# Kernel tuning notes

Measured on AMD Instinct MI355X. Metric: run time of the kernel, lower is better.

The kernel has to match this reference:

```python
import jax, jax.numpy as jnp
import numpy as np

B, N = 16, 63
Np1 = N + 1
M = Np1 * Np1
NB_LABELS = 8
NB_EDGE_LABELS = 4


def _sinkhorn(S, n_iter):
    # LSAPE eps-assignment: alternately normalize rows/cols, leaving the
    # epsilon (last) row/col unnormalized since it may absorb many nodes.
    inner = jnp.arange(Np1) < N
    def step(S, _):
        S = jnp.where(inner[None, :, None], S / S.sum(2, keepdims=True), S)
        S = jnp.where(inner[None, None, :], S / S.sum(1, keepdims=True), S)
        return S, None
    S, _ = jax.lax.scan(step, S, None, length=n_iter)
    return S


def _forward(node_weighs, edge_weighs, A1, A2, l1, l2):
    cn = jax.nn.relu(node_weighs)
    ce = jax.nn.relu(edge_weighs)
    node_ins_del, edge_ins_del = cn[-1], ce[-1]
    iu = jnp.triu_indices(NB_LABELS, k=1)
    node_costs = jnp.zeros((NB_LABELS, NB_LABELS), cn.dtype).at[iu].set(cn[:-1])
    node_costs = node_costs + node_costs.T
    ie = jnp.triu_indices(NB_EDGE_LABELS, k=1)
    edge_costs = jnp.zeros((NB_EDGE_LABELS, NB_EDGE_LABELS), ce.dtype).at[ie].set(ce[:-1])
    edge_costs = edge_costs + edge_costs.T
    E1 = NB_EDGE_LABELS + 1
    # pairwise edge-cost lookup table T[a,b], a,b in {0..E}, 0 = no edge.
    # substitution added twice, matching add_ followed by C = C + ... in source.
    T = jnp.zeros((E1, E1), ce.dtype)
    T = T.at[1:, 1:].set(2.0 * edge_costs)
    T = T.at[0, 1:].set(edge_ins_del)
    T = T.at[1:, 0].set(edge_ins_del)
    # pad adjacency with the epsilon row/col of zeros
    A1p = jnp.pad(A1, ((0, 0), (0, 1), (0, 1)))
    A2p = jnp.pad(A2, ((0, 0), (0, 1), (0, 1)))
    # Dmat[b, u*Np1+v, i*Np1+l] = T[A1p[b,u,i], A2p[b,v,l]]  (quadratic edge term)
    idx = A1p[:, :, None, :, None] * E1 + A2p[:, None, :, None, :]
    Dmat = T.reshape(-1)[idx.reshape(B, M, M)]
    dia = jnp.arange(M)
    Dmat = Dmat.at[:, dia, dia].set(0.0)  # C - eye*diag(C)
    # linear node-cost vector c (diagonal of C): substitution on the N x N
    # block, nodeInsDel on epsilon row/col, 0 at (eps,eps).
    nc = node_costs[l1[:, :, None], l2[:, None, :]]
    cmat = jnp.full((B, Np1, Np1), node_ins_del, node_weighs.dtype)
    cmat = cmat.at[:, :N, :N].set(nc)
    cmat = cmat.at[:, N, N].set(0.0)
    c = cmat.reshape(B, M)
    # eps-assignment init (10 Sinkhorn iters), then Frank-Wolfe (15 iters,
    # 5 Sinkhorn iters per LAP solve), matching franck_wolfe(x0, D, c, 5, 15, n, m).
    x0 = _sinkhorn(jnp.exp(-cmat), 10).reshape(B, M)
    def fw_step(x, _):
        g = c + jnp.einsum('bpq,bq->bp', Dmat, x)
        b = _sinkhorn(jnp.exp(-g.reshape(B, Np1, Np1)), 5).reshape(B, M)
        d = b - x
        den = jnp.einsum('bp,bpq,bq->b', d, Dmat, d)
        num = jnp.einsum('bp,bp->b', d, g)
        t = jnp.where(den > 0.0,
                      jnp.clip(-num / jnp.where(den > 0.0, den, 1.0), 0.0, 1.0),
                      (num < 0.0).astype(x.dtype))
        return x + t[:, None] * d, None
    x, _ = jax.lax.scan(fw_step, x0, None, length=15)
    ged = 0.5 * jnp.einsum('bp,bpq,bq->b', x, Dmat, x) + jnp.einsum('bp,bp->b', c, x)
    return (ged - ged.min()) / (ged.max() - ged.min())


def _sym_adj(key):
    lab = jax.random.randint(key, (B, N, N), 0, NB_EDGE_LABELS + 1)
    keep = jax.random.uniform(jax.random.fold_in(key, 1), (B, N, N)) < 0.15
    A = jnp.triu(lab * keep, 1)
    return (A + jnp.transpose(A, (0, 2, 1))).astype(jnp.int32)


def setup_inputs() -> dict:
    key = jax.random.key(0)
    k = jax.random.split(key, 6)
    n_pairs = NB_LABELS * (NB_LABELS - 1) // 2
    e_pairs = NB_EDGE_LABELS * (NB_EDGE_LABELS - 1) // 2
    base = 1.0 / (n_pairs + e_pairs + 2)
    return {
        'node_weighs': base + 0.001 * jax.random.uniform(k[0], (n_pairs + 1,), jnp.float32),
        'edge_weighs': base + 0.001 * jax.random.uniform(k[1], (e_pairs + 1,), jnp.float32),
        'A1': _sym_adj(k[2]),
        'A2': _sym_adj(k[3]),
        'l1': jax.random.randint(k[4], (B, N), 0, NB_LABELS).astype(jnp.int32),
        'l2': jax.random.randint(k[5], (B, N), 0, NB_LABELS).astype(jnp.int32),
    }


def reference(node_weighs, edge_weighs, A1, A2, l1, l2):
    return _forward(node_weighs, edge_weighs, A1, A2, l1, l2)
```

## Files before the change

### kernel.cpp

```cpp
#include <hip/hip_runtime.h>
#include <math.h>

#define NBATCH 16
#define NN 63

typedef __attribute__((ext_vector_type(8))) short short8;
typedef __attribute__((ext_vector_type(4))) float f32x4;

__device__ __forceinline__ unsigned short f2bf(float f) {
    unsigned int u = __float_as_uint(f);
    u += 0x7fffu + ((u >> 16) & 1u);
    return (unsigned short)(u >> 16);
}

template <int CTRL>
__device__ __forceinline__ float dpp_add(float s) {
    int si = __builtin_bit_cast(int, s);
    int t  = __builtin_amdgcn_update_dpp(si, si, CTRL, 0xF, 0xF, true);
    return s + __builtin_bit_cast(float, t);
}
__device__ __forceinline__ float red8_dpp(float s) {
    s = dpp_add<0xB1>(s);
    s = dpp_add<0x4E>(s);
    s = dpp_add<0x141>(s);
    return s;
}

__global__ __launch_bounds__(512) void ged_kernel(
    const float* __restrict__ node_w, const float* __restrict__ edge_w,
    const int* __restrict__ A1g, const int* __restrict__ A2g,
    const int* __restrict__ l1g, const int* __restrict__ l2g,
    float* __restrict__ ged_out)
{
    const int b    = blockIdx.x;
    const int tid  = threadIdx.x;
    const int lane = tid & 63;
    const int w    = tid >> 6;
    const int lr   = lane & 15;
    const int lg   = lane >> 4;

    __shared__ __align__(16) float XK[64*65];
    __shared__ __align__(16) unsigned short Xb[4096];
    __shared__ __align__(16) unsigned short Rb[4][4096];
    __shared__ __align__(16) unsigned short Wb[4][4096];
    __shared__ __align__(16) unsigned short I1b[4][4096];
    __shared__ __align__(16) float rX[64];
    __shared__ __align__(16) float us[64];
    __shared__ __align__(16) float vs[64];
    __shared__ __align__(16) float red[16];
    __shared__ float ncost[64];
    __shared__ unsigned short Qbf[20];
    __shared__ float cns[29], ces[7];
    __shared__ float deg2f[64];
    __shared__ int l1s[64], l2s[64];

    if (tid < 29) cns[tid] = fmaxf(node_w[tid], 0.f);
    else if (tid >= 32 && tid < 39) ces[tid-32] = fmaxf(edge_w[tid-32], 0.f);
    if (tid >= 64 && tid < 128) l1s[tid-64] = (tid-64 < NN) ? l1g[b*NN + tid-64] : 0;
    else if (tid >= 128 && tid < 192) l2s[tid-128] = (tid-128 < NN) ? l2g[b*NN + tid-128] : 0;
    __syncthreads();
    if (tid < 64) {
        int r0 = tid >> 3, c1 = tid & 7;
        float vv = 0.f;
        if (r0 != c1) {
            int lo = min(r0, c1), hi = max(r0, c1);
            vv = cns[lo*7 - (lo*(lo-1))/2 + (hi-lo-1)];
        }
        ncost[tid] = vv;
    } else if (tid < 80) {
        int a = (tid-64) >> 2, b2 = tid & 3;
        float ec = 0.f;
        if (a != b2) {
            int lo = min(a, b2), hi = max(a, b2);
            ec = ces[lo*3 - (lo*(lo-1))/2 + (hi-lo-1)];
        }
        Qbf[a*5 + b2 + 1] = f2bf(2.f*ec - 2.f*ces[6]);
    } else if (tid < 84) {
        Qbf[(tid-80)*5] = 0;
    }
    __syncthreads();
    #pragma unroll
    for (int r = 0; r < 8; ++r) {
        int row = w + (r << 3);
        int v2 = 0, v1 = 0;
        if (row < NN && lane < NN) {
            v2 = A2g[((size_t)b*NN + row)*NN + lane];
            v1 = A1g[((size_t)b*NN + row)*NN + lane];
        }
        int T = row >> 4, lrr = row & 15;
        int kc = lane >> 5, lgg = (lane >> 3) & 3, e = lane & 7;
        int ci = ((((T<<1)+kc)*4 + lgg)*16 + lrr)*8 + e;
        Wb[0][ci] = Qbf[ 0 + v2];
        Wb[1][ci] = Qbf[ 5 + v2];
        Wb[2][ci] = Qbf[10 + v2];
        Wb[3][ci] = Qbf[15 + v2];
        unsigned long long mv = __ballot(v2 != 0);
        if (lane == 0) deg2f[row] = (float)__popcll(mv);
        I1b[0][ci] = (v1 == 1) ? 0x3F80 : 0;
        I1b[1][ci] = (v1 == 2) ? 0x3F80 : 0;
        I1b[2][ci] = (v1 == 3) ? 0x3F80 : 0;
        I1b[3][ci] = (v1 == 4) ? 0x3F80 : 0;
    }
    __syncthreads();

    const float eid = ces[6];
    const float nid = cns[28];

    int i0s[2], jcs[2], rts[2], cts[2];
    float ed2s[2];
    #pragma unroll
    for (int s = 0; s < 2; ++s) {
        int t = w + (s << 3);
        rts[s] = t >> 2; cts[s] = t & 3;
        i0s[s] = rts[s]*16 + lg*4;
        jcs[s] = cts[s]*16 + lr;
        ed2s[s] = eid * deg2f[jcs[s]];
    }

    float c_reg[2][4];
    #pragma unroll
    for (int s = 0; s < 2; ++s)
        #pragma unroll
        for (int r = 0; r < 4; ++r) {
            int i = i0s[s] + r, j = jcs[s];
            c_reg[s][r] = (i < NN && j < NN) ? ncost[(l1s[i] << 3) + l2s[j]]
                          : ((i == NN && j == NN) ? 0.f : nid);
        }

    const int q8  = tid & 7;
    const int rr8 = tid >> 3;
    const int c8  = q8 << 3;
    float Krow[8], Kcol[8];

    auto expK = [&](float (*gv)[4]) {
        #pragma unroll
        for (int s = 0; s < 2; ++s)
            #pragma unroll
            for (int r = 0; r < 4; ++r)
                XK[(i0s[s] + r)*65 + jcs[s]] = __expf(-gv[s][r]);
        __syncthreads();
    };

    auto sink8 = [&](int iters) {
        #pragma unroll
        for (int u = 0; u < 8; ++u) {
            Krow[u] = XK[rr8*65 + c8 + u];
            Kcol[u] = XK[(c8+u)*65 + rr8];
        }
        float s0 = ((Krow[0]+Krow[1])+(Krow[2]+Krow[3]))+((Krow[4]+Krow[5])+(Krow[6]+Krow[7]));
        s0 = red8_dpp(s0);
        if (q8 == 0) us[rr8] = (rr8 < NN) ? __builtin_amdgcn_rcpf(s0) : 1.f;
        __syncthreads();
        for (int it = 0; it < iters; ++it) {
            {
                float4 ua = *(const float4*)&us[c8], ub = *(const float4*)&us[c8+4];
                float t = ((Kcol[0]*ua.x + Kcol[1]*ua.y) + (Kcol[2]*ua.z + Kcol[3]*ua.w))
                        + ((Kcol[4]*ub.x + Kcol[5]*ub.y) + (Kcol[6]*ub.z + Kcol[7]*ub.w));
                t = red8_dpp(t);
                if (q8 == 0) vs[rr8] = (rr8 < NN) ? __builtin_amdgcn_rcpf(t) : 1.f;
            }
            __syncthreads();
            if (it + 1 < iters) {
                float4 va = *(const float4*)&vs[c8], vb = *(const float4*)&vs[c8+4];
                float t = ((Krow[0]*va.x + Krow[1]*va.y) + (Krow[2]*va.z + Krow[3]*va.w))
                        + ((Krow[4]*vb.x + Krow[5]*vb.y) + (Krow[6]*vb.z + Krow[7]*vb.w));
                t = red8_dpp(t);
                if (q8 == 0) us[rr8] = (rr8 < NN) ? __builtin_amdgcn_rcpf(t) : 1.f;
                __syncthreads();
            }
        }
    };

    auto fin8 = [&]() {
        float4 va = *(const float4*)&vs[c8], vb = *(const float4*)&vs[c8+4];
        float uR = us[rr8];
        float p[8];
        p[0]=Krow[0]*va.x; p[1]=Krow[1]*va.y; p[2]=Krow[2]*va.z; p[3]=Krow[3]*va.w;
        p[4]=Krow[4]*vb.x; p[5]=Krow[5]*vb.y; p[6]=Krow[6]*vb.z; p[7]=Krow[7]*vb.w;
        float sr = red8_dpp(((p[0]+p[1])+(p[2]+p[3])) + ((p[4]+p[5])+(p[6]+p[7])));
        short8 xs;
        #pragma unroll
        for (int u = 0; u < 8; ++u) {
            float xv = uR * p[u];
            XK[rr8*65 + c8 + u] = xv;
            xs[u] = (short)f2bf(xv);
        }
        int ci = (((((rr8>>4)<<1) + (q8>>2))*4 + (q8&3))*16 + (rr8&15)) << 3;
        *(short8*)&Xb[ci] = xs;
        if (q8 == 0) rX[rr8] = uR * sr;
        __syncthreads();
    };

    auto M1R = [&]() {
        #pragma unroll
        for (int s = 0; s < 2; ++s) {
            const int rt = rts[s], ct = cts[s];
            f32x4 P0 = {0.f,0.f,0.f,0.f}, P1 = P0, P2 = P0, P3 = P0;
            #pragma unroll
            for (int kc = 0; kc < 2; ++kc) {
                const int ai = ((((rt<<1)+kc)*4 + lg)*16 + lr) << 3;
                const int bi = ((((ct<<1)+kc)*4 + lg)*16 + lr) << 3;
                short8 af = *(const short8*)&Xb[ai];
                P0 = __builtin_amdgcn_mfma_f32_16x16x32_bf16(af, *(const short8*)&Wb[0][bi], P0, 0,0,0);
                P1 = __builtin_amdgcn_mfma_f32_16x16x32_bf16(af, *(const short8*)&Wb[1][bi], P1, 0,0,0);
                P2 = __builtin_amdgcn_mfma_f32_16x16x32_bf16(af, *(const short8*)&Wb[2][bi], P2, 0,0,0);
                P3 = __builtin_amdgcn_mfma_f32_16x16x32_bf16(af, *(const short8*)&Wb[3][bi], P3, 0,0,0);
            }
            float4 rx4 = *(const float4*)&rX[i0s[s]];
            P0[0] += eid*rx4.x; P0[1] += eid*rx4.y; P0[2] += eid*rx4.z; P0[3] += eid*rx4.w;
            P1[0] += eid*rx4.x; P1[1] += eid*rx4.y; P1[2] += eid*rx4.z; P1[3] += eid*rx4.w;
            P2[0] += eid*rx4.x; P2[1] += eid*rx4.y; P2[2] += eid*rx4.z; P2[3] += eid*rx4.w;
            P3[0] += eid*rx4.x; P3[1] += eid*rx4.y; P3[2] += eid*rx4.z; P3[3] += eid*rx4.w;
            const int cw = (((ct<<1) + (rt>>1))*4 + ((rt&1)*2 + (lg>>1)))*16 + lr;
            const int si = (cw << 3) + ((lg & 1) << 2);
            {
                unsigned long long v =  (unsigned long long)(f2bf(P0[0]) | ((unsigned)f2bf(P0[1])<<16))
                                     | ((unsigned long long)(f2bf(P0[2]) | ((unsigned)f2bf(P0[3])<<16)) << 32);
                *(unsigned long long*)&Rb[0][si] = v;
            }
            {
                unsigned long long v =  (unsigned long long)(f2bf(P1[0]) | ((unsigned)f2bf(P1[1])<<16))
                                     | ((unsigned long long)(f2bf(P1[2]) | ((unsigned)f2bf(P1[3])<<16)) << 32);
                *(unsigned long long*)&Rb[1][si] = v;
            }
            {
                unsigned long long v =  (unsigned long long)(f2bf(P2[0]) | ((unsigned)f2bf(P2[1])<<16))
                                     | ((unsigned long long)(f2bf(P2[2]) | ((unsigned)f2bf(P2[3])<<16)) << 32);
                *(unsigned long long*)&Rb[2][si] = v;
            }
            {
                unsigned long long v =  (unsigned long long)(f2bf(P3[0]) | ((unsigned)f2bf(P3[1])<<16))
                                     | ((unsigned long long)(f2bf(P3[2]) | ((unsigned)f2bf(P3[3])<<16)) << 32);
                *(unsigned long long*)&Rb[3][si] = v;
            }
        }
        __syncthreads();
    };

    auto M2 = [&](float (*out)[4]) {
        #pragma unroll
        for (int s = 0; s < 2; ++s) {
            const int rt = rts[s], ct = cts[s];
            f32x4 acc = {0.f,0.f,0.f,0.f};
            #pragma unroll
            for (int kc = 0; kc < 2; ++kc) {
                const int ai = ((((rt<<1)+kc)*4 + lg)*16 + lr) << 3;
                const int bi = ((((ct<<1)+kc)*4 + lg)*16 + lr) << 3;
                #pragma unroll
                for (int a = 0; a < 4; ++a) {
                    short8 af = *(const short8*)&I1b[a][ai];
                    short8 bf = *(const short8*)&Rb[a][bi];
                    acc = __builtin_amdgcn_mfma_f32_16x16x32_bf16(af, bf, acc, 0,0,0);
                }
            }
            #pragma unroll
            for (int r = 0; r < 4; ++r) out[s][r] = acc[r] + ed2s[s];
        }
    };

    expK(c_reg);
    sink8(10);
    fin8();
    M1R();
    float x[2][4], dx[2][4], bb[2][4], gvv[2][4];
    M2(dx);
    #pragma unroll
    for (int s = 0; s < 2; ++s)
        #pragma unroll
        for (int r = 0; r < 4; ++r)
            x[s][r] = XK[(i0s[s] + r)*65 + jcs[s]];

    for (int it = 0; it < 15; ++it) {
        #pragma unroll
        for (int s = 0; s < 2; ++s)
            #pragma unroll
            for (int r = 0; r < 4; ++r)
                gvv[s][r] = c_reg[s][r] + dx[s][r];
        expK(gvv);
        sink8(5);
        fin8();
        M1R();
        float db[2][4];
        M2(db);
        #pragma unroll
        for (int s = 0; s < 2; ++s)
            #pragma unroll
            for (int r = 0; r < 4; ++r)
                bb[s][r] = XK[(i0s[s] + r)*65 + jcs[s]];
        float dn = 0.f, nm = 0.f;
        #pragma unroll
        for (int s = 0; s < 2; ++s)
            #pragma unroll
            for (int r = 0; r < 4; ++r) {
                float d = bb[s][r] - x[s][r];
                dn += d * (db[s][r] - dx[s][r]);
                nm += d * gvv[s][r];
            }
        dn = red8_dpp(dn);  nm = red8_dpp(nm);
        dn += __shfl_xor(dn, 8, 64);  nm += __shfl_xor(nm, 8, 64);
        dn += __shfl_xor(dn, 16, 64); nm += __shfl_xor(nm, 16, 64);
        dn += __shfl_xor(dn, 32, 64); nm += __shfl_xor(nm, 32, 64);
        if (lane == 0) { red[w] = dn; red[8 + w] = nm; }
        __syncthreads();
        float4 pa = *(const float4*)&red[0], pb = *(const float4*)&red[4];
        float4 pc = *(const float4*)&red[8], pd = *(const float4*)&red[12];
        float den = (pa.x+pa.y+pa.z+pa.w) + (pb.x+pb.y+pb.z+pb.w);
        float num = (pc.x+pc.y+pc.z+pc.w) + (pd.x+pd.y+pd.z+pd.w);
        float t;
        if (den > 0.f) t = fminf(fmaxf(-num / den, 0.f), 1.f);
        else           t = (num < 0.f) ? 1.f : 0.f;
        #pragma unroll
        for (int s = 0; s < 2; ++s)
            #pragma unroll
            for (int r = 0; r < 4; ++r) {
                float d = bb[s][r] - x[s][r];
                x[s][r]  += t * d;
                dx[s][r] += t * (db[s][r] - dx[s][r]);
            }
    }

    __syncthreads();
    float g2 = 0.f;
    #pragma unroll
    for (int s = 0; s < 2; ++s)
        #pragma unroll
        for (int r = 0; r < 4; ++r)
            g2 += x[s][r] * (0.5f * dx[s][r] + c_reg[s][r]);
    g2 = red8_dpp(g2);
    g2 += __shfl_xor(g2, 8, 64);
    g2 += __shfl_xor(g2, 16, 64);
    g2 += __shfl_xor(g2, 32, 64);
    if (lane == 0) red[w] = g2;
    __syncthreads();
    if (tid == 0) {
        float s = 0.f;
        #pragma unroll
        for (int u = 0; u < 8; ++u) s += red[u];
        ged_out[b] = s;
    }
}

__global__ void norm_kernel(const float* __restrict__ g, float* __restrict__ out) {
    int t = threadIdx.x;
    if (t < NBATCH) {
        float mn = g[0], mx = g[0];
        #pragma unroll
        for (int i = 1; i < NBATCH; ++i) { mn = fminf(mn, g[i]); mx = fmaxf(mx, g[i]); }
        out[t] = (g[t] - mn) / (mx - mn);
    }
}

extern "C" void kernel_launch(void* const* d_in, const int* in_sizes, int n_in,
                              void* d_out, int out_size, void* d_ws, size_t ws_size,
                              hipStream_t stream) {
    (void)in_sizes; (void)n_in; (void)out_size; (void)ws_size;
    const float* node_w = (const float*)d_in[0];
    const float* edge_w = (const float*)d_in[1];
    const int*   A1     = (const int*)d_in[2];
    const int*   A2     = (const int*)d_in[3];
    const int*   l1     = (const int*)d_in[4];
    const int*   l2     = (const int*)d_in[5];
    float* ged = (float*)d_ws;
    ged_kernel<<<dim3(NBATCH), dim3(512), 0, stream>>>(node_w, edge_w, A1, A2, l1, l2, ged);
    norm_kernel<<<dim3(1), dim3(64), 0, stream>>>(ged, (float*)d_out);
}
```

Before: 80.13 us.

## Run Sinkhorn iterations in a single wavefront to eliminate block barriers

The Sinkhorn row/column normalization loop moves from all 8 wavefronts, which needed a block-wide barrier after every half-step, to wavefront 0 alone. Each lane of that wavefront holds a full 64-wide row and column of K in registers, using a transposed shared copy XKT written during the exp step. The intent is to remove the many __syncthreads per Frank-Wolfe iteration in exchange for serial 64-element dot products per lane, with the other 7 waves idle during that phase. Padding changes to 68 so the row accesses can use aligned float4 loads, and the finalize step is vectorized to match.

Measured after the change: 131.6 us. 1.64x slower.

```diff
diff --git a/kernel.cpp b/kernel.cpp
--- a/kernel.cpp
+++ b/kernel.cpp
@@ -3,6 +3,7 @@
 
 #define NBATCH 16
 #define NN 63
+#define XS 68
 
 typedef __attribute__((ext_vector_type(8))) short short8;
 typedef __attribute__((ext_vector_type(4))) float f32x4;
@@ -39,7 +40,8 @@
     const int lr   = lane & 15;
     const int lg   = lane >> 4;
 
-    __shared__ __align__(16) float XK[64*65];
+    __shared__ __align__(16) float XK[64*XS];
+    __shared__ __align__(16) float XKT[64*XS];
     __shared__ __align__(16) unsigned short Xb[4096];
     __shared__ __align__(16) unsigned short Rb[4][4096];
     __shared__ __align__(16) unsigned short Wb[4][4096];
@@ -130,61 +132,74 @@
     const int q8  = tid & 7;
     const int rr8 = tid >> 3;
     const int c8  = q8 << 3;
-    float Krow[8], Kcol[8];
 
     auto expK = [&](float (*gv)[4]) {
         #pragma unroll
         for (int s = 0; s < 2; ++s)
             #pragma unroll
-            for (int r = 0; r < 4; ++r)
-                XK[(i0s[s] + r)*65 + jcs[s]] = __expf(-gv[s][r]);
-        __syncthreads();
-    };
-
-    auto sink8 = [&](int iters) {
-        #pragma unroll
-        for (int u = 0; u < 8; ++u) {
-            Krow[u] = XK[rr8*65 + c8 + u];
-            Kcol[u] = XK[(c8+u)*65 + rr8];
-        }
-        float s0 = ((Krow[0]+Krow[1])+(Krow[2]+Krow[3]))+((Krow[4]+Krow[5])+(Krow[6]+Krow[7]));
-        s0 = red8_dpp(s0);
-        if (q8 == 0) us[rr8] = (rr8 < NN) ? __builtin_amdgcn_rcpf(s0) : 1.f;
-        __syncthreads();
-        for (int it = 0; it < iters; ++it) {
-            {
-                float4 ua = *(const float4*)&us[c8], ub = *(const float4*)&us[c8+4];
-                float t = ((Kcol[0]*ua.x + Kcol[1]*ua.y) + (Kcol[2]*ua.z + Kcol[3]*ua.w))
-                        + ((Kcol[4]*ub.x + Kcol[5]*ub.y) + (Kcol[6]*ub.z + Kcol[7]*ub.w));
-                t = red8_dpp(t);
-                if (q8 == 0) vs[rr8] = (rr8 < NN) ? __builtin_amdgcn_rcpf(t) : 1.f;
-            }
-            __syncthreads();
-            if (it + 1 < iters) {
-                float4 va = *(const float4*)&vs[c8], vb = *(const float4*)&vs[c8+4];
-                float t = ((Krow[0]*va.x + Krow[1]*va.y) + (Krow[2]*va.z + Krow[3]*va.w))
-                        + ((Krow[4]*vb.x + Krow[5]*vb.y) + (Krow[6]*vb.z + Krow[7]*vb.w));
-                t = red8_dpp(t);
-                if (q8 == 0) us[rr8] = (rr8 < NN) ? __builtin_amdgcn_rcpf(t) : 1.f;
-                __syncthreads();
-            }
-        }
-    };
-
-    auto fin8 = [&]() {
-        float4 va = *(const float4*)&vs[c8], vb = *(const float4*)&vs[c8+4];
+            for (int r = 0; r < 4; ++r) {
+                float e = __expf(-gv[s][r]);
+                XK [(i0s[s] + r)*XS + jcs[s]] = e;
+                XKT[jcs[s]*XS + (i0s[s] + r)] = e;
+            }
+        __syncthreads();
+    };
+
+    auto sinkW0 = [&](int iters) {
+        if (w == 0) {
+            f32x4 Kr[16], Kc[16];
+            #pragma unroll
+            for (int u = 0; u < 16; ++u) {
+                Kr[u] = *(const f32x4*)&XK [lane*XS + (u << 2)];
+                Kc[u] = *(const f32x4*)&XKT[lane*XS + (u << 2)];
+            }
+            float s0 = 0.f;
+            #pragma unroll
+            for (int u = 0; u < 16; ++u)
+                s0 += (Kr[u][0] + Kr[u][1]) + (Kr[u][2] + Kr[u][3]);
+            us[lane] = (lane < NN) ? __builtin_amdgcn_rcpf(s0) : 1.f;
+            for (int it = 0; it < iters; ++it) {
+                float t = 0.f;
+                #pragma unroll
+                for (int u = 0; u < 16; ++u) {
+                    f32x4 uu = *(const f32x4*)&us[u << 2];
+                    t += (Kc[u][0]*uu[0] + Kc[u][1]*uu[1])
+                       + (Kc[u][2]*uu[2] + Kc[u][3]*uu[3]);
+                }
+                vs[lane] = (lane < NN) ? __builtin_amdgcn_rcpf(t) : 1.f;
+                if (it + 1 < iters) {
+                    float t2 = 0.f;
+                    #pragma unroll
+                    for (int u = 0; u < 16; ++u) {
+                        f32x4 vv = *(const f32x4*)&vs[u << 2];
+                        t2 += (Kr[u][0]*vv[0] + Kr[u][1]*vv[1])
+                            + (Kr[u][2]*vv[2] + Kr[u][3]*vv[3]);
+                    }
+                    us[lane] = (lane < NN) ? __builtin_amdgcn_rcpf(t2) : 1.f;
+                }
+            }
+        }
+        __syncthreads();
+    };
+
+    auto fin8all = [&]() {
+        f32x4 k0 = *(const f32x4*)&XK[rr8*XS + c8];
+        f32x4 k1 = *(const f32x4*)&XK[rr8*XS + c8 + 4];
+        f32x4 va = *(const f32x4*)&vs[c8];
+        f32x4 vb = *(const f32x4*)&vs[c8 + 4];
         float uR = us[rr8];
-        float p[8];
-        p[0]=Krow[0]*va.x; p[1]=Krow[1]*va.y; p[2]=Krow[2]*va.z; p[3]=Krow[3]*va.w;
-        p[4]=Krow[4]*vb.x; p[5]=Krow[5]*vb.y; p[6]=Krow[6]*vb.z; p[7]=Krow[7]*vb.w;
-        float sr = red8_dpp(((p[0]+p[1])+(p[2]+p[3])) + ((p[4]+p[5])+(p[6]+p[7])));
+        float p0 = k0[0]*va[0], p1 = k0[1]*va[1], p2 = k0[2]*va[2], p3 = k0[3]*va[3];
+        float p4 = k1[0]*vb[0], p5 = k1[1]*vb[1], p6 = k1[2]*vb[2], p7 = k1[3]*vb[3];
+        float sr = red8_dpp(((p0+p1)+(p2+p3)) + ((p4+p5)+(p6+p7)));
+        f32x4 xa = {uR*p0, uR*p1, uR*p2, uR*p3};
+        f32x4 xb2 = {uR*p4, uR*p5, uR*p6, uR*p7};
+        *(f32x4*)&XK[rr8*XS + c8]     = xa;
+        *(f32x4*)&XK[rr8*XS + c8 + 4] = xb2;
         short8 xs;
-        #pragma unroll
-        for (int u = 0; u < 8; ++u) {
-            float xv = uR * p[u];
-            XK[rr8*65 + c8 + u] = xv;
-            xs[u] = (short)f2bf(xv);
-        }
+        xs[0] = (short)f2bf(xa[0]); xs[1] = (short)f2bf(xa[1]);
+        xs[2] = (short)f2bf(xa[2]); xs[3] = (short)f2bf(xa[3]);
+        xs[4] = (short)f2bf(xb2[0]); xs[5] = (short)f2bf(xb2[1]);
+        xs[6] = (short)f2bf(xb2[2]); xs[7] = (short)f2bf(xb2[3]);
         int ci = (((((rr8>>4)<<1) + (q8>>2))*4 + (q8&3))*16 + (rr8&15)) << 3;
         *(short8*)&Xb[ci] = xs;
         if (q8 == 0) rX[rr8] = uR * sr;
@@ -206,11 +221,11 @@
                 P2 = __builtin_amdgcn_mfma_f32_16x16x32_bf16(af, *(const short8*)&Wb[2][bi], P2, 0,0,0);
                 P3 = __builtin_amdgcn_mfma_f32_16x16x32_bf16(af, *(const short8*)&Wb[3][bi], P3, 0,0,0);
             }
-            float4 rx4 = *(const float4*)&rX[i0s[s]];
-            P0[0] += eid*rx4.x; P0[1] += eid*rx4.y; P0[2] += eid*rx4.z; P0[3] += eid*rx4.w;
-            P1[0] += eid*rx4.x; P1[1] += eid*rx4.y; P1[2] += eid*rx4.z; P1[3] += eid*rx4.w;
-            P2[0] += eid*rx4.x; P2[1] += eid*rx4.y; P2[2] += eid*rx4.z; P2[3] += eid*rx4.w;
-            P3[0] += eid*rx4.x; P3[1] += eid*rx4.y; P3[2] += eid*rx4.z; P3[3] += eid*rx4.w;
+            f32x4 rx4 = *(const f32x4*)&rX[i0s[s]];
+            P0[0] += eid*rx4[0]; P0[1] += eid*rx4[1]; P0[2] += eid*rx4[2]; P0[3] += eid*rx4[3];
+            P1[0] += eid*rx4[0]; P1[1] += eid*rx4[1]; P1[2] += eid*rx4[2]; P1[3] += eid*rx4[3];
+            P2[0] += eid*rx4[0]; P2[1] += eid*rx4[1]; P2[2] += eid*rx4[2]; P2[3] += eid*rx4[3];
+            P3[0] += eid*rx4[0]; P3[1] += eid*rx4[1]; P3[2] += eid*rx4[2]; P3[3] += eid*rx4[3];
             const int cw = (((ct<<1) + (rt>>1))*4 + ((rt&1)*2 + (lg>>1)))*16 + lr;
             const int si = (cw << 3) + ((lg & 1) << 2);
             {
@@ -259,8 +274,8 @@
     };
 
     expK(c_reg);
-    sink8(10);
-    fin8();
+    sinkW0(10);
+    fin8all();
     M1R();
     float x[2][4], dx[2][4], bb[2][4], gvv[2][4];
     M2(dx);
@@ -268,7 +283,7 @@
     for (int s = 0; s < 2; ++s)
         #pragma unroll
         for (int r = 0; r < 4; ++r)
-            x[s][r] = XK[(i0s[s] + r)*65 + jcs[s]];
+            x[s][r] = XK[(i0s[s] + r)*XS + jcs[s]];
 
     for (int it = 0; it < 15; ++it) {
         #pragma unroll
@@ -277,8 +292,8 @@
             for (int r = 0; r < 4; ++r)
                 gvv[s][r] = c_reg[s][r] + dx[s][r];
         expK(gvv);
-        sink8(5);
-        fin8();
+        sinkW0(5);
+        fin8all();
         M1R();
         float db[2][4];
         M2(db);
@@ -286,7 +301,7 @@
         for (int s = 0; s < 2; ++s)
             #pragma unroll
             for (int r = 0; r < 4; ++r)
-                bb[s][r] = XK[(i0s[s] + r)*65 + jcs[s]];
+                bb[s][r] = XK[(i0s[s] + r)*XS + jcs[s]];
         float dn = 0.f, nm = 0.f;
         #pragma unroll
         for (int s = 0; s < 2; ++s)
@@ -302,10 +317,10 @@
         dn += __shfl_xor(dn, 32, 64); nm += __shfl_xor(nm, 32, 64);
         if (lane == 0) { red[w] = dn; red[8 + w] = nm; }
         __syncthreads();
-        float4 pa = *(const float4*)&red[0], pb = *(const float4*)&red[4];
-        float4 pc = *(const float4*)&red[8], pd = *(const float4*)&red[12];
-        float den = (pa.x+pa.y+pa.z+pa.w) + (pb.x+pb.y+pb.z+pb.w);
-        float num = (pc.x+pc.y+pc.z+pc.w) + (pd.x+pd.y+pd.z+pd.w);
+        f32x4 pa = *(const f32x4*)&red[0], pb = *(const f32x4*)&red[4];
+        f32x4 pc = *(const f32x4*)&red[8], pd = *(const f32x4*)&red[12];
+        float den = (pa[0]+pa[1]+pa[2]+pa[3]) + (pb[0]+pb[1]+pb[2]+pb[3]);
+        float num = (pc[0]+pc[1]+pc[2]+pc[3]) + (pd[0]+pd[1]+pd[2]+pd[3]);
         float t;
         if (den > 0.f) t = fminf(fmaxf(-num / den, 0.f), 1.f);
         else           t = (num < 0.f) ? 1.f : 0.f;
```
